# Kernel optimization log

Hardware: AMD Instinct MI355X
Metric: run time of the kernel (lower is better)

The kernel has to match this reference:

```python
import jax, jax.numpy as jnp
import numpy as np

B, LQ, LK, D, NH = 16, 1024, 1024, 160, 8
HD = D // NH
EPS = 1e-5


def _ln(x, g, b):
    m = x.mean(-1, keepdims=True)
    v = ((x - m) ** 2).mean(-1, keepdims=True)
    return (x - m) / jnp.sqrt(v + EPS) * g + b


def _heads(x, L):
    # [B,L,D] -> [B,NH,L,HD]
    return x.reshape(B, L, NH, HD).transpose(0, 2, 1, 3)


def _attn(qh, kh, vh, scale):
    logits = jnp.einsum('bhqd,bhkd->bhqk', qh, kh) * scale
    p = jax.nn.softmax(logits, axis=-1)
    o = jnp.einsum('bhqk,bhkd->bhqd', p, vh)
    return o.transpose(0, 2, 1, 3).reshape(B, -1, D)


def setup_inputs() -> dict:
    key = jax.random.key(0)
    ks = jax.random.split(key, 16)
    s = 0.02
    inp = {
        'q': jax.random.normal(ks[0], (B, LQ, D), jnp.float32),
        'kv': jax.random.normal(ks[1], (B, LK, D), jnp.float32),
        'ln1_g': jnp.ones((D,), jnp.float32), 'ln1_b': jnp.zeros((D,), jnp.float32),
        'sa_in_w': jax.random.normal(ks[2], (3 * D, D), jnp.float32) * s,
        'sa_in_b': jnp.zeros((3 * D,), jnp.float32),
        'sa_out_w': jax.random.normal(ks[3], (D, D), jnp.float32) * s,
        'sa_out_b': jnp.zeros((D,), jnp.float32),
        'ln2_g': jnp.ones((D,), jnp.float32), 'ln2_b': jnp.zeros((D,), jnp.float32),
        'lnkv_g': jnp.ones((D,), jnp.float32), 'lnkv_b': jnp.zeros((D,), jnp.float32),
        'ca_qw': jax.random.normal(ks[4], (D, D), jnp.float32) * s,
        'ca_qb': jnp.zeros((D,), jnp.float32),
        'ca_kw': jax.random.normal(ks[5], (D, D), jnp.float32) * s,
        'ca_kb': jnp.zeros((D,), jnp.float32),
        'ca_vw': jax.random.normal(ks[6], (D, D), jnp.float32) * s,
        'ca_vb': jnp.zeros((D,), jnp.float32),
        'ca_ow': jax.random.normal(ks[7], (D, D), jnp.float32) * s,
        'ca_ob': jnp.zeros((D,), jnp.float32),
        'log_tau': jnp.zeros((1,), jnp.float32),
        'lnf_g': jnp.ones((D,), jnp.float32), 'lnf_b': jnp.zeros((D,), jnp.float32),
        'w1': jax.random.normal(ks[8], (4 * D, D), jnp.float32) * s,
        'b1': jnp.zeros((4 * D,), jnp.float32),
        'w2': jax.random.normal(ks[9], (D, 4 * D), jnp.float32) * s,
        'b2': jnp.zeros((D,), jnp.float32),
    }
    return inp


def reference(q, kv, ln1_g, ln1_b, sa_in_w, sa_in_b, sa_out_w, sa_out_b,
              ln2_g, ln2_b, lnkv_g, lnkv_b, ca_qw, ca_qb, ca_kw, ca_kb,
              ca_vw, ca_vb, ca_ow, ca_ob, log_tau, lnf_g, lnf_b,
              w1, b1, w2, b2):
    # --- self-attention (pre-LN), standard 1/sqrt(hd) scale ---
    qn = _ln(q, ln1_g, ln1_b)
    qkv = qn @ sa_in_w.T + sa_in_b  # [B,LQ,3D]
    sq, sk, sv = jnp.split(qkv, 3, axis=-1)
    sa = _attn(_heads(sq, LQ), _heads(sk, LQ), _heads(sv, LQ), HD ** -0.5)
    sa = sa @ sa_out_w.T + sa_out_b
    q = q + sa  # DropPath is identity in eval

    # --- cross-attention with learnable temperature ---
    qn = _ln(q, ln2_g, ln2_b)
    kvn = _ln(kv, lnkv_g, lnkv_b)
    tau = jnp.minimum(jax.nn.softplus(log_tau) + 0.5, 2.0)  # clamp max=2.0
    scale = (HD ** -0.5) / tau[0]
    qh = _heads(qn @ ca_qw.T + ca_qb, LQ)
    kh = _heads(kvn @ ca_kw.T + ca_kb, LK)
    vh = _heads(kvn @ ca_vw.T + ca_vb, LK)
    ca = _attn(qh, kh, vh, scale) @ ca_ow.T + ca_ob
    q = q + ca

    # --- FFN with exact GELU ---
    h = _ln(q, lnf_g, lnf_b) @ w1.T + b1
    h = jax.nn.gelu(h, approximate=False)
    q = q + (h @ w2.T + b2)
    return q
```

## Files before the change

### kernel.cpp

```cpp
#include <hip/hip_runtime.h>
#include <hip/hip_bf16.h>
#include <math.h>

#define LQN 1024
#define LKN 1024
#define NB 16
#define DM 160
#define NHEADS 8
#define HDIM 20

typedef __attribute__((ext_vector_type(8))) short bf16x8;
typedef __attribute__((ext_vector_type(4))) float f32x4;

__device__ __forceinline__ float bf2f(unsigned short h) {
  union { unsigned int u; float f; } c; c.u = ((unsigned int)h) << 16; return c.f;
}
__device__ __forceinline__ unsigned short f2bf(float f) {
  union { float f; unsigned int u; } c; c.f = f;
  unsigned int lsb = (c.u >> 16) & 1u;
  unsigned int r = c.u + 0x7fffu + lsb;
  return (unsigned short)(r >> 16);
}
__device__ __forceinline__ unsigned int cvtpk(float a, float b) {
  unsigned int r;
  asm("v_cvt_pk_bf16_f32 %0, %1, %2" : "=v"(r) : "v"(a), "v"(b));
  return r;
}
__device__ __forceinline__ float ex2(float x) { return __builtin_amdgcn_exp2f(x); }

struct CvtArgs {
  const float* src[8];
  int cum[9];
};

__global__ void init_kernel(uint4* __restrict__ zbase, int nz,
                            uint4* __restrict__ vbase, int nv,
                            const float* __restrict__ b0,
                            const float* __restrict__ b1,
                            const float* __restrict__ b2,
                            float* __restrict__ bcat,
                            CvtArgs a, unsigned short* __restrict__ wdst) {
  int i = blockIdx.x * 256 + threadIdx.x;
  if (i < nz) zbase[i] = make_uint4(0, 0, 0, 0);
  if (i < nv) {
    unsigned int v = ((i & 31) == 20) ? 0x3F803F80u : 0u;
    vbase[i] = make_uint4(v, v, v, v);
  }
  if (i < 480) bcat[i] = (i < 160) ? b0[i] : (i < 320 ? b1[i - 160] : b2[i - 320]);
  if (i < 409600) {
    int s = 0;
#pragma unroll
    for (int t = 0; t < 7; ++t) s += (i >= a.cum[t + 1]) ? 1 : 0;
    wdst[i] = f2bf(a.src[s][i - a.cum[s]]);
  }
}

__global__ void ln_kernel(const float* __restrict__ x,
                          const float* __restrict__ g,
                          const float* __restrict__ b,
                          unsigned short* __restrict__ y, int rows) {
  int row = blockIdx.x * 4 + (threadIdx.x >> 6);
  int lane = threadIdx.x & 63;
  const float* xr = x + (size_t)row * DM;
  float a0 = xr[lane];
  float a1 = xr[lane + 64];
  float a2 = (lane < 32) ? xr[lane + 128] : 0.0f;
  float s = a0 + a1 + a2;
#pragma unroll
  for (int m = 1; m < 64; m <<= 1) s += __shfl_xor(s, m);
  float mean = s * (1.0f / DM);
  float d0 = a0 - mean, d1 = a1 - mean, d2 = a2 - mean;
  float vs = d0 * d0 + d1 * d1 + ((lane < 32) ? d2 * d2 : 0.0f);
#pragma unroll
  for (int m = 1; m < 64; m <<= 1) vs += __shfl_xor(vs, m);
  float rstd = rsqrtf(vs * (1.0f / DM) + 1e-5f);
  unsigned short* yr = y + (size_t)row * DM;
  yr[lane]      = f2bf(d0 * rstd * g[lane]      + b[lane]);
  yr[lane + 64] = f2bf(d1 * rstd * g[lane + 64] + b[lane + 64]);
  if (lane < 32)
    yr[lane + 128] = f2bf(d2 * rstd * g[lane + 128] + b[lane + 128]);
}

__global__ void ln2_kernel(const float* __restrict__ x1,
                           const float* __restrict__ g1,
                           const float* __restrict__ b1,
                           unsigned short* __restrict__ y1,
                           const float* __restrict__ x2,
                           const float* __restrict__ g2,
                           const float* __restrict__ b2,
                           unsigned short* __restrict__ y2, int rowsPer) {
  int row = blockIdx.x * 4 + (threadIdx.x >> 6);
  int lane = threadIdx.x & 63;
  const float* x; const float* g; const float* b; unsigned short* y;
  if (row < rowsPer) {
    x = x1 + (size_t)row * DM; g = g1; b = b1; y = y1 + (size_t)row * DM;
  } else {
    int r2 = row - rowsPer;
    x = x2 + (size_t)r2 * DM; g = g2; b = b2; y = y2 + (size_t)r2 * DM;
  }
  float a0 = x[lane];
  float a1 = x[lane + 64];
  float a2 = (lane < 32) ? x[lane + 128] : 0.0f;
  float s = a0 + a1 + a2;
#pragma unroll
  for (int m = 1; m < 64; m <<= 1) s += __shfl_xor(s, m);
  float mean = s * (1.0f / DM);
  float d0 = a0 - mean, d1 = a1 - mean, d2 = a2 - mean;
  float vs = d0 * d0 + d1 * d1 + ((lane < 32) ? d2 * d2 : 0.0f);
#pragma unroll
  for (int m = 1; m < 64; m <<= 1) vs += __shfl_xor(vs, m);
  float rstd = rsqrtf(vs * (1.0f / DM) + 1e-5f);
  y[lane]      = f2bf(d0 * rstd * g[lane]      + b[lane]);
  y[lane + 64] = f2bf(d1 * rstd * g[lane + 64] + b[lane + 64]);
  if (lane < 32)
    y[lane + 128] = f2bf(d2 * rstd * g[lane + 128] + b[lane + 128]);
}

template <int EPI, int NCOL>
__global__ __launch_bounds__(256, 2)
void gemm160_kernel(const unsigned short* __restrict__ Aq,
                    const unsigned short* __restrict__ Akv,
                    const unsigned short* __restrict__ W,
                    const float* __restrict__ bias,
                    const float* __restrict__ res,
                    void* __restrict__ outp,
                    unsigned short* __restrict__ Kc,
                    unsigned short* __restrict__ Vc) {
  __shared__ unsigned short wl[NCOL * 16 * 168];
  int tid = threadIdx.x;
  int lane = tid & 63;
  int w = tid >> 6;
  int y = blockIdx.y;
  const unsigned short* Wb = W + y * (NCOL * 2560);
  for (int idx = tid * 8; idx < NCOL * 2560; idx += 2048) {
    int col = idx / 160, k = idx % 160;
    *(uint4*)(wl + col * 168 + k) = *(const uint4*)(Wb + idx);
  }
  __syncthreads();
  int lr = lane & 15;
  int g = lane >> 4;
  int R0 = blockIdx.x * 64;
  int rbase = R0 + w * 16;
  const unsigned short* A = (EPI == 0 && y > 0) ? Akv : Aq;
  const unsigned short* Ap = A + (size_t)(rbase + lr) * 160 + g * 8;
  const unsigned short* wp = wl + lr * 168 + g * 8;
  f32x4 acc[NCOL];
#pragma unroll
  for (int c = 0; c < NCOL; ++c) acc[c] = (f32x4){0, 0, 0, 0};
#pragma unroll
  for (int k0 = 0; k0 < 160; k0 += 32) {
    bf16x8 a = *(const bf16x8*)(Ap + k0);
#pragma unroll
    for (int c = 0; c < NCOL; ++c) {
      bf16x8 bfr = *(const bf16x8*)(wp + c * 16 * 168 + k0);
      acc[c] = __builtin_amdgcn_mfma_f32_16x16x32_bf16(a, bfr, acc[c], 0, 0, 0);
    }
  }
  if (EPI == 0) {
    if (y == 0) {
      unsigned short* Qp = (unsigned short*)outp;
#pragma unroll
      for (int c = 0; c < NCOL; ++c) {
        int col = c * 16 + lr;
        int h = col / 20, d = col % 20;
        float bc = bias[col];
#pragma unroll
        for (int r = 0; r < 4; ++r) {
          int row = rbase + g * 4 + r;
          Qp[(size_t)row * 256 + h * 32 + d] = f2bf(acc[c][r] + bc);
        }
      }
    } else if (y == 1) {
      int b = R0 >> 10;
#pragma unroll
      for (int c = 0; c < NCOL; ++c) {
        int col = c * 16 + lr;
        int h = col / 20, d = col % 20;
        float bc = bias[160 + col];
        size_t base = ((((size_t)(b * 8 + h)) * 4 + (d >> 3)) * 1024) * 8 + (d & 7);
#pragma unroll
        for (int r = 0; r < 4; ++r) {
          int tok = (rbase + g * 4 + r) & 1023;
          Kc[base + (size_t)tok * 8] = f2bf(acc[c][r] + bc);
        }
      }
    } else {
      int b = R0 >> 10;
      int base64 = R0 & 1023;
      int slotbase = base64 + g * 8 + (w & 1) * 4 + (w >> 1) * 32;
#pragma unroll
      for (int c = 0; c < NCOL; ++c) {
        int col = c * 16 + lr;
        int h = col / 20, d = col % 20;
        float bc = bias[320 + col];
        size_t vb = ((size_t)(b * 8 + h) * 128) * 256 + (size_t)d * 8;
#pragma unroll
        for (int r = 0; r < 4; ++r) {
          int S = slotbase + r;
          Vc[vb + (size_t)(S >> 3) * 256 + (S & 7)] = f2bf(acc[c][r] + bc);
        }
      }
    }
  } else if (EPI == 1) {
    float* out = (float*)outp;
#pragma unroll
    for (int c = 0; c < NCOL; ++c) {
      int gcol = y * NCOL * 16 + c * 16 + lr;
      float bc = bias[gcol];
#pragma unroll
      for (int r = 0; r < 4; ++r) {
        int row = rbase + g * 4 + r;
        out[(size_t)row * 160 + gcol] = acc[c][r] + bc + res[(size_t)row * 160 + gcol];
      }
    }
  } else {
    unsigned short* out = (unsigned short*)outp;
#pragma unroll
    for (int c = 0; c < NCOL; ++c) {
      int colg = y * NCOL * 16 + c * 16 + lr;
      float bc = bias[colg];
#pragma unroll
      for (int r = 0; r < 4; ++r) {
        int row = rbase + g * 4 + r;
        float v = acc[c][r] + bc;
        v = 0.5f * v * (1.0f + erff(v * 0.70710678118654752f));
        out[(size_t)row * 640 + colg] = f2bf(v);
      }
    }
  }
}

template <int K>
__global__ __launch_bounds__(256, 4)
void gemm_kernel(const unsigned short* __restrict__ A,
                 const unsigned short* __restrict__ W,
                 const float* __restrict__ bias,
                 const float* __restrict__ res,
                 float* __restrict__ out, int N) {
  int lane = threadIdx.x & 63;
  int wid = threadIdx.x >> 6;
  int wr = wid >> 1, wc = wid & 1;
  int r0 = blockIdx.x * 64 + wr * 32;
  int c0 = blockIdx.y * 64 + wc * 32;
  if (c0 >= N) return;
  int lr = lane & 15;
  int ko = (lane >> 4) * 8;
  const unsigned short* Ap0 = A + (size_t)(r0 + lr) * K + ko;
  const unsigned short* Ap1 = Ap0 + (size_t)16 * K;
  const unsigned short* Wp0 = W + (size_t)(c0 + lr) * K + ko;
  const unsigned short* Wp1 = Wp0 + (size_t)16 * K;
  f32x4 acc00 = {0, 0, 0, 0}, acc01 = {0, 0, 0, 0};
  f32x4 acc10 = {0, 0, 0, 0}, acc11 = {0, 0, 0, 0};
#pragma unroll
  for (int k = 0; k < K; k += 32) {
    bf16x8 a0 = *(const bf16x8*)(Ap0 + k);
    bf16x8 a1 = *(const bf16x8*)(Ap1 + k);
    bf16x8 b0 = *(const bf16x8*)(Wp0 + k);
    bf16x8 b1 = *(const bf16x8*)(Wp1 + k);
    acc00 = __builtin_amdgcn_mfma_f32_16x16x32_bf16(a0, b0, acc00, 0, 0, 0);
    acc01 = __builtin_amdgcn_mfma_f32_16x16x32_bf16(a0, b1, acc01, 0, 0, 0);
    acc10 = __builtin_amdgcn_mfma_f32_16x16x32_bf16(a1, b0, acc10, 0, 0, 0);
    acc11 = __builtin_amdgcn_mfma_f32_16x16x32_bf16(a1, b1, acc11, 0, 0, 0);
  }
  int cA = c0 + lr, cB = c0 + 16 + lr;
  float bc0 = bias[cA];
  float bc1 = bias[cB];
  int rb = (lane >> 4) * 4;
#pragma unroll
  for (int i = 0; i < 2; ++i) {
    f32x4 aA = i ? acc10 : acc00;
    f32x4 aB = i ? acc11 : acc01;
#pragma unroll
    for (int r = 0; r < 4; ++r) {
      int row = r0 + i * 16 + rb + r;
      out[(size_t)row * N + cA] = aA[r] + bc0 + res[(size_t)row * N + cA];
      out[(size_t)row * N + cB] = aB[r] + bc1 + res[(size_t)row * N + cB];
    }
  }
}

__global__ __launch_bounds__(256, 4)
void attn_kernel(const unsigned short* __restrict__ Qp,
                 const unsigned short* __restrict__ Kc,
                 const unsigned short* __restrict__ Vc,
                 unsigned short* __restrict__ O,
                 const float* __restrict__ tau_ptr,
                 float base_scale) {
  __shared__ unsigned short kbuf[2][4096];
  __shared__ unsigned short vbuf[2][4096];
  int lane = threadIdx.x & 63;
  int wid = threadIdx.x >> 6;
  int bh = blockIdx.x;
  int b = bh >> 3, h = bh & 7;
  int q0 = blockIdx.y * 128 + wid * 32;
  float sc = base_scale;
  if (tau_ptr) {
    float lt = tau_ptr[0];
    float sp = (lt > 20.0f) ? lt : log1pf(expf(lt));
    sc /= fminf(sp + 0.5f, 2.0f);
  }
  float scale = sc * 1.4426950408889634f;
  int lr = lane & 15;
  int g = lane >> 4;
  int ko = g * 8;
  int rb = g * 4;
  const size_t tb = (size_t)b * LQN;
  union { bf16x8 v; unsigned short s[8]; unsigned int u[4]; } fq0, fq1;
  fq0.v = *(const bf16x8*)(Qp + (tb + q0 + lr) * 256 + h * 32 + ko);
  fq1.v = *(const bf16x8*)(Qp + (tb + q0 + 16 + lr) * 256 + h * 32 + ko);
#pragma unroll
  for (int j = 0; j < 4; ++j) {
    fq0.u[j] = cvtpk(bf2f(fq0.s[2 * j]) * scale, bf2f(fq0.s[2 * j + 1]) * scale);
    fq1.u[j] = cvtpk(bf2f(fq1.s[2 * j]) * scale, bf2f(fq1.s[2 * j + 1]) * scale);
  }
  bf16x8 aq0 = fq0.v, aq1 = fq1.v;
  const unsigned short* ksrc = Kc + (((size_t)bh * 4 + wid) * 1024) * 8;
  const unsigned short* vsrc = Vc + (size_t)bh * 32768;
  int sd = wid * 1024 + lane * 8;
  {
    uint4 k0 = *(const uint4*)(ksrc + lane * 8);
    uint4 k1 = *(const uint4*)(ksrc + (64 + lane) * 8);
    uint4 v0 = *(const uint4*)(vsrc + sd);
    uint4 v1 = *(const uint4*)(vsrc + sd + 512);
    *(uint4*)(kbuf[0] + sd) = k0;
    *(uint4*)(kbuf[0] + sd + 512) = k1;
    *(uint4*)(vbuf[0] + sd) = v0;
    *(uint4*)(vbuf[0] + sd + 512) = v1;
  }
  __syncthreads();
  int cur = 0;
  f32x4 o00 = {0, 0, 0, 0}, o01 = {0, 0, 0, 0};
  f32x4 o10 = {0, 0, 0, 0}, o11 = {0, 0, 0, 0};
  const f32x4 zero = {0, 0, 0, 0};

#define ATTN_COMPUTE(KB, VB)                                                   \
  {                                                                            \
    const unsigned short* kp_ = (KB);                                          \
    const unsigned short* vp_ = (VB);                                          \
    bf16x8 ck0 = *(const bf16x8*)(kp_ + g * 1024 + lr * 8);                    \
    bf16x8 ck1 = *(const bf16x8*)(kp_ + g * 1024 + (16 + lr) * 8);             \
    bf16x8 ck2 = *(const bf16x8*)(kp_ + g * 1024 + (32 + lr) * 8);             \
    bf16x8 ck3 = *(const bf16x8*)(kp_ + g * 1024 + (48 + lr) * 8);             \
    f32x4 s0 = __builtin_amdgcn_mfma_f32_16x16x32_bf16(ck0, aq0, zero, 0, 0, 0);\
    f32x4 s1 = __builtin_amdgcn_mfma_f32_16x16x32_bf16(ck1, aq0, zero, 0, 0, 0);\
    f32x4 s2 = __builtin_amdgcn_mfma_f32_16x16x32_bf16(ck2, aq0, zero, 0, 0, 0);\
    f32x4 s3 = __builtin_amdgcn_mfma_f32_16x16x32_bf16(ck3, aq0, zero, 0, 0, 0);\
    union { bf16x8 v; unsigned int u[4]; } p1, p2, p3, p4;                     \
    p1.u[0] = cvtpk(ex2(s0[0]), ex2(s0[1]));                                   \
    p1.u[1] = cvtpk(ex2(s0[2]), ex2(s0[3]));                                   \
    p1.u[2] = cvtpk(ex2(s1[0]), ex2(s1[1]));                                   \
    p1.u[3] = cvtpk(ex2(s1[2]), ex2(s1[3]));                                   \
    p2.u[0] = cvtpk(ex2(s2[0]), ex2(s2[1]));                                   \
    p2.u[1] = cvtpk(ex2(s2[2]), ex2(s2[3]));                                   \
    p2.u[2] = cvtpk(ex2(s3[0]), ex2(s3[1]));                                   \
    p2.u[3] = cvtpk(ex2(s3[2]), ex2(s3[3]));                                   \
    s0 = __builtin_amdgcn_mfma_f32_16x16x32_bf16(ck0, aq1, zero, 0, 0, 0);     \
    s1 = __builtin_amdgcn_mfma_f32_16x16x32_bf16(ck1, aq1, zero, 0, 0, 0);     \
    s2 = __builtin_amdgcn_mfma_f32_16x16x32_bf16(ck2, aq1, zero, 0, 0, 0);     \
    s3 = __builtin_amdgcn_mfma_f32_16x16x32_bf16(ck3, aq1, zero, 0, 0, 0);     \
    p3.u[0] = cvtpk(ex2(s0[0]), ex2(s0[1]));                                   \
    p3.u[1] = cvtpk(ex2(s0[2]), ex2(s0[3]));                                   \
    p3.u[2] = cvtpk(ex2(s1[0]), ex2(s1[1]));                                   \
    p3.u[3] = cvtpk(ex2(s1[2]), ex2(s1[3]));                                   \
    p4.u[0] = cvtpk(ex2(s2[0]), ex2(s2[1]));                                   \
    p4.u[1] = cvtpk(ex2(s2[2]), ex2(s2[3]));                                   \
    p4.u[2] = cvtpk(ex2(s3[0]), ex2(s3[1]));                                   \
    p4.u[3] = cvtpk(ex2(s3[2]), ex2(s3[3]));                                   \
    bf16x8 w00 = *(const bf16x8*)(vp_ + g * 256 + lr * 8);                     \
    bf16x8 w01 = *(const bf16x8*)(vp_ + (4 + g) * 256 + lr * 8);               \
    bf16x8 w10 = *(const bf16x8*)(vp_ + g * 256 + (16 + lr) * 8);              \
    bf16x8 w11 = *(const bf16x8*)(vp_ + (4 + g) * 256 + (16 + lr) * 8);        \
    o00 = __builtin_amdgcn_mfma_f32_16x16x32_bf16(p1.v, w00, o00, 0, 0, 0);    \
    o00 = __builtin_amdgcn_mfma_f32_16x16x32_bf16(p2.v, w01, o00, 0, 0, 0);    \
    o01 = __builtin_amdgcn_mfma_f32_16x16x32_bf16(p1.v, w10, o01, 0, 0, 0);    \
    o01 = __builtin_amdgcn_mfma_f32_16x16x32_bf16(p2.v, w11, o01, 0, 0, 0);    \
    o10 = __builtin_amdgcn_mfma_f32_16x16x32_bf16(p3.v, w00, o10, 0, 0, 0);    \
    o10 = __builtin_amdgcn_mfma_f32_16x16x32_bf16(p4.v, w01, o10, 0, 0, 0);    \
    o11 = __builtin_amdgcn_mfma_f32_16x16x32_bf16(p3.v, w10, o11, 0, 0, 0);    \
    o11 = __builtin_amdgcn_mfma_f32_16x16x32_bf16(p4.v, w11, o11, 0, 0, 0);    \
  }

#pragma unroll 1
  for (int kt = 0; kt < LKN; kt += 128) {
    int ktn = (kt + 128 < LKN) ? kt + 128 : 0;
    uint4 kA0 = *(const uint4*)(ksrc + (ktn + lane) * 8);
    uint4 kA1 = *(const uint4*)(ksrc + (ktn + 64 + lane) * 8);
    uint4 vA0 = *(const uint4*)(vsrc + ktn * 32 + sd);
    uint4 vA1 = *(const uint4*)(vsrc + ktn * 32 + sd + 512);
    ATTN_COMPUTE(kbuf[cur], vbuf[cur])
    *(uint4*)(kbuf[cur ^ 1] + sd) = kA0;
    *(uint4*)(kbuf[cur ^ 1] + sd + 512) = kA1;
    ATTN_COMPUTE(kbuf[cur] + 512, vbuf[cur] + 2048)
    *(uint4*)(vbuf[cur ^ 1] + sd) = vA0;
    *(uint4*)(vbuf[cur ^ 1] + sd + 512) = vA1;
    __syncthreads();
    cur ^= 1;
  }
#undef ATTN_COMPUTE
  unsigned short* ob = O + (tb + q0) * DM + h * HDIM;
  int psl = (lane & 48) + 4;
#pragma unroll
  for (int r = 0; r < 4; ++r) {
    int qr = rb + r;
    float inv0 = 1.0f / __shfl(o01[r], psl, 64);
    ob[(size_t)qr * DM + lr] = f2bf(o00[r] * inv0);
    if (lr < 4) ob[(size_t)qr * DM + 16 + lr] = f2bf(o01[r] * inv0);
    float inv1 = 1.0f / __shfl(o11[r], psl, 64);
    ob[(size_t)(16 + qr) * DM + lr] = f2bf(o10[r] * inv1);
    if (lr < 4) ob[(size_t)(16 + qr) * DM + 16 + lr] = f2bf(o11[r] * inv1);
  }
}

extern "C" void kernel_launch(void* const* d_in, const int* in_sizes, int n_in,
                              void* d_out, int out_size, void* d_ws, size_t ws_size,
                              hipStream_t stream) {
  (void)in_sizes; (void)n_in; (void)out_size; (void)ws_size;
  const float* q        = (const float*)d_in[0];
  const float* kv       = (const float*)d_in[1];
  const float* ln1_g    = (const float*)d_in[2];
  const float* ln1_b    = (const float*)d_in[3];
  const float* sa_in_w  = (const float*)d_in[4];
  const float* sa_in_b  = (const float*)d_in[5];
  const float* sa_out_w = (const float*)d_in[6];
  const float* sa_out_b = (const float*)d_in[7];
  const float* ln2_g    = (const float*)d_in[8];
  const float* ln2_b    = (const float*)d_in[9];
  const float* lnkv_g   = (const float*)d_in[10];
  const float* lnkv_b   = (const float*)d_in[11];
  const float* ca_qw    = (const float*)d_in[12];
  const float* ca_qb    = (const float*)d_in[13];
  const float* ca_kw    = (const float*)d_in[14];
  const float* ca_kb    = (const float*)d_in[15];
  const float* ca_vw    = (const float*)d_in[16];
  const float* ca_vb    = (const float*)d_in[17];
  const float* ca_ow    = (const float*)d_in[18];
  const float* ca_ob    = (const float*)d_in[19];
  const float* log_tau  = (const float*)d_in[20];
  const float* lnf_g    = (const float*)d_in[21];
  const float* lnf_b    = (const float*)d_in[22];
  const float* w1       = (const float*)d_in[23];
  const float* b1       = (const float*)d_in[24];
  const float* w2       = (const float*)d_in[25];
  const float* b2       = (const float*)d_in[26];

  const int M = NB * LQN;
  char* ws = (char*)d_ws;
  unsigned short* wb   = (unsigned short*)(ws);
  float*          bcat = (float*)(ws + 860160);
  unsigned short* qn   = (unsigned short*)(ws + 1048576);
  unsigned short* sqp  = (unsigned short*)(ws + 6291456);
  unsigned short* skc  = (unsigned short*)(ws + 14680064);
  unsigned short* svc  = (unsigned short*)(ws + 23068672);
  unsigned short* attn = (unsigned short*)(ws + 31457280);
  unsigned short* kvn  = (unsigned short*)(ws + 36700160);
  float*          q1   = (float*)(ws + 41943040);
  float*          q2   = (float*)(ws + 52428800);
  unsigned short* hbuf = (unsigned short*)(ws + 6291456);

  unsigned short* b_sa_in  = wb;
  unsigned short* b_sa_out = wb + 76800;
  unsigned short* b_ca_q   = wb + 102400;
  unsigned short* b_ca_o   = wb + 179200;
  unsigned short* b_w1     = wb + 204800;
  unsigned short* b_w2     = wb + 307200;

  dim3 blk(256);
  const float isq = 0.22360679774997896f;

  CvtArgs ca;
  ca.src[0] = sa_in_w;  ca.src[1] = sa_out_w; ca.src[2] = ca_qw; ca.src[3] = ca_kw;
  ca.src[4] = ca_vw;    ca.src[5] = ca_ow;    ca.src[6] = w1;    ca.src[7] = w2;
  int cum[9] = {0, 76800, 102400, 128000, 153600, 179200, 204800, 307200, 409600};
  for (int i = 0; i < 9; ++i) ca.cum[i] = cum[i];
  init_kernel<<<dim3(4096), blk, 0, stream>>>(
      (uint4*)(ws + 6291456), 1048576, (uint4*)(ws + 23068672), 524288,
      ca_qb, ca_kb, ca_vb, bcat, ca, wb);

  ln_kernel<<<dim3(M / 4), blk, 0, stream>>>(q, ln1_g, ln1_b, qn, M);
  gemm160_kernel<0, 10><<<dim3(M / 64, 3), blk, 0, stream>>>(
      qn, qn, b_sa_in, sa_in_b, nullptr, sqp, skc, svc);
  attn_kernel<<<dim3(NB * NHEADS, LQN / 128), blk, 0, stream>>>(sqp, skc, svc, attn, nullptr, isq);
  gemm160_kernel<1, 5><<<dim3(M / 64, 2), blk, 0, stream>>>(
      attn, attn, b_sa_out, sa_out_b, q, q1, nullptr, nullptr);

  ln2_kernel<<<dim3(M / 2), blk, 0, stream>>>(q1, ln2_g, ln2_b, qn,
                                              kv, lnkv_g, lnkv_b, kvn, M);
  gemm160_kernel<0, 10><<<dim3(M / 64, 3), blk, 0, stream>>>(
      qn, kvn, b_ca_q, bcat, nullptr, sqp, skc, svc);
  attn_kernel<<<dim3(NB * NHEADS, LQN / 128), blk, 0, stream>>>(sqp, skc, svc, attn, log_tau, isq);
  gemm160_kernel<1, 5><<<dim3(M / 64, 2), blk, 0, stream>>>(
      attn, attn, b_ca_o, ca_ob, q1, q2, nullptr, nullptr);

  ln_kernel<<<dim3(M / 4), blk, 0, stream>>>(q2, lnf_g, lnf_b, qn, M);
  gemm160_kernel<2, 10><<<dim3(M / 64, 4), blk, 0, stream>>>(
      qn, qn, b_w1, b1, nullptr, hbuf, nullptr, nullptr);
  gemm_kernel<640><<<dim3(M / 64, 3), blk, 0, stream>>>(hbuf, b_w2, b2, q2, (float*)d_out, 160);
}
```

Baseline: 171.6 us.

## Fuse LayerNorm into out-projection GEMM epilogues and merge input LNs

The attention out-projection GEMMs now compute all 160 columns per block (NCOL=10, one grid column), so the epilogue can add bias and residual and then run the following LayerNorm in-register via shuffles, writing the bf16 normalized rows directly. The standalone LN kernels before cross-attention and before the FFN are removed, and the kv LayerNorm is moved up into the first LN launch alongside ln1. This removes two kernel launches and a round trip of the residual stream through global memory. In exchange the out-projection grid shrinks from two column blocks to one, and variance is computed as E[x²]−mean², which is less numerically stable.

```diff
diff --git a/kernel.cpp b/kernel.cpp
--- a/kernel.cpp
+++ b/kernel.cpp
@@ -53,32 +53,6 @@
     for (int t = 0; t < 7; ++t) s += (i >= a.cum[t + 1]) ? 1 : 0;
     wdst[i] = f2bf(a.src[s][i - a.cum[s]]);
   }
-}
-
-__global__ void ln_kernel(const float* __restrict__ x,
-                          const float* __restrict__ g,
-                          const float* __restrict__ b,
-                          unsigned short* __restrict__ y, int rows) {
-  int row = blockIdx.x * 4 + (threadIdx.x >> 6);
-  int lane = threadIdx.x & 63;
-  const float* xr = x + (size_t)row * DM;
-  float a0 = xr[lane];
-  float a1 = xr[lane + 64];
-  float a2 = (lane < 32) ? xr[lane + 128] : 0.0f;
-  float s = a0 + a1 + a2;
-#pragma unroll
-  for (int m = 1; m < 64; m <<= 1) s += __shfl_xor(s, m);
-  float mean = s * (1.0f / DM);
-  float d0 = a0 - mean, d1 = a1 - mean, d2 = a2 - mean;
-  float vs = d0 * d0 + d1 * d1 + ((lane < 32) ? d2 * d2 : 0.0f);
-#pragma unroll
-  for (int m = 1; m < 64; m <<= 1) vs += __shfl_xor(vs, m);
-  float rstd = rsqrtf(vs * (1.0f / DM) + 1e-5f);
-  unsigned short* yr = y + (size_t)row * DM;
-  yr[lane]      = f2bf(d0 * rstd * g[lane]      + b[lane]);
-  yr[lane + 64] = f2bf(d1 * rstd * g[lane + 64] + b[lane + 64]);
-  if (lane < 32)
-    yr[lane + 128] = f2bf(d2 * rstd * g[lane + 128] + b[lane + 128]);
 }
 
 __global__ void ln2_kernel(const float* __restrict__ x1,
@@ -125,7 +99,9 @@
                     const float* __restrict__ res,
                     void* __restrict__ outp,
                     unsigned short* __restrict__ Kc,
-                    unsigned short* __restrict__ Vc) {
+                    unsigned short* __restrict__ Vc,
+                    const float* __restrict__ lng,
+                    const float* __restrict__ lnb) {
   __shared__ unsigned short wl[NCOL * 16 * 168];
   int tid = threadIdx.x;
   int lane = tid & 63;
@@ -201,19 +177,7 @@
         }
       }
     }
-  } else if (EPI == 1) {
-    float* out = (float*)outp;
-#pragma unroll
-    for (int c = 0; c < NCOL; ++c) {
-      int gcol = y * NCOL * 16 + c * 16 + lr;
-      float bc = bias[gcol];
-#pragma unroll
-      for (int r = 0; r < 4; ++r) {
-        int row = rbase + g * 4 + r;
-        out[(size_t)row * 160 + gcol] = acc[c][r] + bc + res[(size_t)row * 160 + gcol];
-      }
-    }
-  } else {
+  } else if (EPI == 2) {
     unsigned short* out = (unsigned short*)outp;
 #pragma unroll
     for (int c = 0; c < NCOL; ++c) {
@@ -225,6 +189,38 @@
         float v = acc[c][r] + bc;
         v = 0.5f * v * (1.0f + erff(v * 0.70710678118654752f));
         out[(size_t)row * 640 + colg] = f2bf(v);
+      }
+    }
+  } else {
+    float* out = (float*)outp;
+#pragma unroll
+    for (int c = 0; c < NCOL; ++c) {
+      int col = c * 16 + lr;
+      float bc = bias[col];
+#pragma unroll
+      for (int r = 0; r < 4; ++r) {
+        int row = rbase + g * 4 + r;
+        float v = acc[c][r] + bc + res[(size_t)row * 160 + col];
+        acc[c][r] = v;
+        out[(size_t)row * 160 + col] = v;
+      }
+    }
+#pragma unroll
+    for (int r = 0; r < 4; ++r) {
+      float s = 0.0f, sq = 0.0f;
+#pragma unroll
+      for (int c = 0; c < NCOL; ++c) { s += acc[c][r]; sq += acc[c][r] * acc[c][r]; }
+#pragma unroll
+      for (int m = 1; m < 16; m <<= 1) { s += __shfl_xor(s, m); sq += __shfl_xor(sq, m); }
+      float mean = s * (1.0f / DM);
+      float var = sq * (1.0f / DM) - mean * mean;
+      float rstd = rsqrtf(var + 1e-5f);
+      int row = rbase + g * 4 + r;
+#pragma unroll
+      for (int c = 0; c < NCOL; ++c) {
+        int col = c * 16 + lr;
+        Kc[(size_t)row * 160 + col] =
+            f2bf((acc[c][r] - mean) * rstd * lng[col] + lnb[col]);
       }
     }
   }
@@ -476,23 +472,22 @@
       (uint4*)(ws + 6291456), 1048576, (uint4*)(ws + 23068672), 524288,
       ca_qb, ca_kb, ca_vb, bcat, ca, wb);
 
-  ln_kernel<<<dim3(M / 4), blk, 0, stream>>>(q, ln1_g, ln1_b, qn, M);
+  ln2_kernel<<<dim3(M / 2), blk, 0, stream>>>(q, ln1_g, ln1_b, qn,
+                                              kv, lnkv_g, lnkv_b, kvn, M);
+
   gemm160_kernel<0, 10><<<dim3(M / 64, 3), blk, 0, stream>>>(
-      qn, qn, b_sa_in, sa_in_b, nullptr, sqp, skc, svc);
+      qn, qn, b_sa_in, sa_in_b, nullptr, sqp, skc, svc, nullptr, nullptr);
   attn_kernel<<<dim3(NB * NHEADS, LQN / 128), blk, 0, stream>>>(sqp, skc, svc, attn, nullptr, isq);
-  gemm160_kernel<1, 5><<<dim3(M / 64, 2), blk, 0, stream>>>(
-      attn, attn, b_sa_out, sa_out_b, q, q1, nullptr, nullptr);
-
-  ln2_kernel<<<dim3(M / 2), blk, 0, stream>>>(q1, ln2_g, ln2_b, qn,
-                                              kv, lnkv_g, lnkv_b, kvn, M);
+  gemm160_kernel<3, 10><<<dim3(M / 64, 1), blk, 0, stream>>>(
+      attn, attn, b_sa_out, sa_out_b, q, q1, qn, nullptr, ln2_g, ln2_b);
+
   gemm160_kernel<0, 10><<<dim3(M / 64, 3), blk, 0, stream>>>(
-      qn, kvn, b_ca_q, bcat, nullptr, sqp, skc, svc);
+      qn, kvn, b_ca_q, bcat, nullptr, sqp, skc, svc, nullptr, nullptr);
   attn_kernel<<<dim3(NB * NHEADS, LQN / 128), blk, 0, stream>>>(sqp, skc, svc, attn, log_tau, isq);
-  gemm160_kernel<1, 5><<<dim3(M / 64, 2), blk, 0, stream>>>(
-      attn, attn, b_ca_o, ca_ob, q1, q2, nullptr, nullptr);
-
-  ln_kernel<<<dim3(M / 4), blk, 0, stream>>>(q2, lnf_g, lnf_b, qn, M);
+  gemm160_kernel<3, 10><<<dim3(M / 64, 1), blk, 0, stream>>>(
+      attn, attn, b_ca_o, ca_ob, q1, q2, qn, nullptr, lnf_g, lnf_b);
+
   gemm160_kernel<2, 10><<<dim3(M / 64, 4), blk, 0, stream>>>(
-      qn, qn, b_w1, b1, nullptr, hbuf, nullptr, nullptr);
+      qn, qn, b_w1, b1, nullptr, hbuf, nullptr, nullptr, nullptr, nullptr);
   gemm_kernel<640><<<dim3(M / 64, 3), blk, 0, stream>>>(hbuf, b_w2, b2, q2, (float*)d_out, 160);
 }
```

Result: faster. 168.1 us (-2.0%).
